# Performance work log

Hardware: AMD Instinct MI355X
Metric: run time of the kernel (lower is better)

Reference implementation:

```python
import jax, jax.numpy as jnp
import numpy as np

DT = 0.01
OMEGA_MAX = 100.0


def setup_inputs() -> dict:
    key = jax.random.key(0)
    ks = jax.random.split(key, 7)
    B, T, D, M = 4, 4096, 1024, 64
    N = 2 * M
    u = jax.random.normal(ks[0], (B, T, D), dtype=jnp.float32)
    W_omega = jax.random.normal(ks[1], (M, D), dtype=jnp.float32) * 0.02
    b_omega = jnp.ones((M,), dtype=jnp.float32)
    W_zeta = jax.random.normal(ks[2], (M, D), dtype=jnp.float32) * 0.02
    b_zeta = jnp.zeros((M,), dtype=jnp.float32)
    W_B = jax.random.normal(ks[3], (N, D), dtype=jnp.float32) * (0.1 / np.sqrt(D))
    b_B = jnp.zeros((N,), dtype=jnp.float32)
    C = jax.random.normal(ks[4], (D, N), dtype=jnp.float32) * 0.01
    D_mat = jax.random.normal(ks[5], (D, D), dtype=jnp.float32) * 0.01
    return dict(u=u, W_omega=W_omega, b_omega=b_omega, W_zeta=W_zeta,
                b_zeta=b_zeta, W_B=W_B, b_B=b_B, C=C, D_mat=D_mat)


def reference(u, W_omega, b_omega, W_zeta, b_zeta, W_B, b_B, C, D_mat):
    B, T, D = u.shape
    M = W_omega.shape[0]
    # Hoist all per-step linear projections into batched GEMMs (same math).
    omega = jax.nn.softplus(jnp.einsum('btd,md->btm', u, W_omega) + b_omega)
    omega = jnp.clip(omega, 1e-4, OMEGA_MAX)                      # (B,T,M)
    zeta = jax.nn.sigmoid(jnp.einsum('btd,md->btm', u, W_zeta) + b_zeta)
    A = omega * omega                                             # (B,T,M)
    S = 1.0 / (1.0 + (DT * DT) * A)                               # (B,T,M)
    d = 1.0 - zeta                                                # (B,T,M)
    F = jnp.einsum('btd,nd->btn', u, W_B) + b_B                   # (B,T,2M)

    def step(x, inp):
        A_t, S_t, d_t, F_t = inp                                  # (B,M)x3, (B,2M)
        z = x[:, :M]
        y = x[:, M:]
        z_new = d_t * (S_t * z - DT * A_t * S_t * y)
        y_new = d_t * (DT * S_t * z + S_t * y)
        x_new = jnp.concatenate([z_new, y_new], axis=-1) + F_t
        return x_new, x_new

    x0 = jnp.zeros((B, 2 * M), dtype=u.dtype)
    tm = lambda a: jnp.swapaxes(a, 0, 1)  # to time-major for scan
    _, xs = jax.lax.scan(step, x0, (tm(A), tm(S), tm(d), tm(F)))
    xs = jnp.swapaxes(xs, 0, 1)                                   # (B,T,2M)
    # Output projection: y_t = x_t C^T + u_t D^T
    y = jnp.einsum('btn,dn->btd', xs, C) + jnp.einsum('bte,de->btd', u, D_mat)
    return y
```

## Files before the change

kernel.cpp:

```cpp
#include <hip/hip_runtime.h>
#include <hip/hip_bf16.h>
#include <math.h>

#define DTC 0.01f

typedef __attribute__((ext_vector_type(8))) short short8;
typedef __attribute__((ext_vector_type(4))) float f32x4;
typedef unsigned short bf16raw;

__device__ __forceinline__ bf16raw f2bf(float f){
  union { unsigned u; float f; } v; v.f = f;
  unsigned r = v.u + 0x7FFF + ((v.u >> 16) & 1u);
  return (bf16raw)(r >> 16);
}

__device__ __forceinline__ short8 ld8f(const float* __restrict__ p){
  float4 a = *(const float4*)p;
  float4 b = *(const float4*)(p + 4);
  short8 r;
  r[0] = (short)f2bf(a.x); r[1] = (short)f2bf(a.y);
  r[2] = (short)f2bf(a.z); r[3] = (short)f2bf(a.w);
  r[4] = (short)f2bf(b.x); r[5] = (short)f2bf(b.y);
  r[6] = (short)f2bf(b.z); r[7] = (short)f2bf(b.w);
  return r;
}

template<int ITERS>
__device__ __forceinline__ void stage_async(const bf16raw* __restrict__ src, long ld,
                                            long row0, int k0, bf16raw* lds,
                                            int wave, int lane){
  int kchunk = (lane & 3) ^ ((lane >> 3) & 3);
#pragma unroll
  for (int i = 0; i < ITERS; ++i){
    int r0 = (wave*ITERS + i) * 16;
    long row = row0 + r0 + (lane >> 2);
    const bf16raw* gp = src + row*ld + k0 + kchunk*8;
    bf16raw* lp = lds + r0*32;
    __builtin_amdgcn_global_load_lds((const __attribute__((address_space(1))) void*)gp,
                                     (__attribute__((address_space(3))) void*)lp,
                                     16, 0, 0);
  }
}

template<int MI, int NI>
__device__ __forceinline__ void mma_tile(const bf16raw* Alds, const bf16raw* Blds,
                                         f32x4 acc[MI][NI], int wm, int wn, int quad, int t16){
  short8 af[MI], bfr[NI];
  int sw = (quad ^ ((t16 >> 1) & 3)) * 8;
#pragma unroll
  for (int mi = 0; mi < MI; ++mi)
    af[mi] = *(const short8*)(Alds + (wm*(MI*16) + mi*16 + t16)*32 + sw);
#pragma unroll
  for (int ni = 0; ni < NI; ++ni)
    bfr[ni] = *(const short8*)(Blds + (wn*(NI*16) + ni*16 + t16)*32 + sw);
#pragma unroll
  for (int mi = 0; mi < MI; ++mi)
#pragma unroll
    for (int ni = 0; ni < NI; ++ni)
      acc[mi][ni] = __builtin_amdgcn_mfma_f32_16x16x32_bf16(af[mi], bfr[ni], acc[mi][ni], 0, 0, 0);
}

extern "C" __global__ void k_prep(const float* __restrict__ u,
    const float* __restrict__ Wom, const float* __restrict__ Wze,
    const float* __restrict__ WB, const float* __restrict__ Cm,
    const float* __restrict__ Dm, bf16raw* __restrict__ u_bf,
    bf16raw* __restrict__ Wcat, bf16raw* __restrict__ C_bf,
    bf16raw* __restrict__ Dm_bf){
  for (long g = (long)blockIdx.x * 256 + threadIdx.x; g < 2277376;
       g += (long)gridDim.x * 256){
    const float* src; bf16raw* dst; long o;
    if      (g < 2097152){ src = u;   dst = u_bf;          o = g; }
    else if (g < 2105344){ src = Wom; dst = Wcat;          o = g - 2097152; }
    else if (g < 2113536){ src = Wze; dst = Wcat + 65536;  o = g - 2105344; }
    else if (g < 2129920){ src = WB;  dst = Wcat + 131072; o = g - 2113536; }
    else if (g < 2146304){ src = Cm;  dst = C_bf;          o = g - 2129920; }
    else                 { src = Dm;  dst = Dm_bf;         o = g - 2146304; }
    *(short8*)(dst + o*8) = ld8f(src + o*8);
  }
}

extern "C" __global__ __launch_bounds__(256, 4) void k_gemm_p(
    const bf16raw* __restrict__ u_bf, const bf16raw* __restrict__ Wcat,
    float* __restrict__ P){
  __shared__ __align__(16) bf16raw Alds[3*64*32];
  __shared__ __align__(16) bf16raw Blds[3*64*32];
  int tid = threadIdx.x, wave = tid >> 6, lane = tid & 63;
  int quad = lane >> 4, t16 = lane & 15;
  int wm = wave >> 1, wn = wave & 1;
  int id  = blockIdx.y * gridDim.x + blockIdx.x;
  int sid = (id & 7) * 128 + (id >> 3);
  long row0 = (long)(sid >> 2) * 64;
  int  col0 = (sid & 3) * 64;
  f32x4 acc[2][2] = {};

  auto stage = [&](int kt, int buf){
    stage_async<1>(u_bf, 1024, row0, kt*32, Alds + buf*(64*32), wave, lane);
    stage_async<1>(Wcat, 1024, col0, kt*32, Blds + buf*(64*32), wave, lane);
  };

  stage(0, 0);
  stage(1, 1);
  int rd = 0;
  for (int s = 0; s < 30; ++s){
    asm volatile("s_waitcnt vmcnt(2)" ::: "memory");
    __builtin_amdgcn_s_barrier();
    __builtin_amdgcn_sched_barrier(0);
    int st = rd >= 1 ? rd - 1 : 2;
    stage(s + 2, st);
    __builtin_amdgcn_s_setprio(1);
    mma_tile<2,2>(Alds + rd*(64*32), Blds + rd*(64*32), acc, wm, wn, quad, t16);
    __builtin_amdgcn_s_setprio(0);
    rd = rd < 2 ? rd + 1 : 0;
  }
  asm volatile("s_waitcnt vmcnt(2)" ::: "memory");
  __builtin_amdgcn_s_barrier();
  __builtin_amdgcn_sched_barrier(0);
  mma_tile<2,2>(Alds + 0*(64*32), Blds + 0*(64*32), acc, wm, wn, quad, t16);
  asm volatile("s_waitcnt vmcnt(0)" ::: "memory");
  __builtin_amdgcn_s_barrier();
  __builtin_amdgcn_sched_barrier(0);
  mma_tile<2,2>(Alds + 1*(64*32), Blds + 1*(64*32), acc, wm, wn, quad, t16);
#pragma unroll
  for (int mi = 0; mi < 2; ++mi)
#pragma unroll
    for (int ni = 0; ni < 2; ++ni)
#pragma unroll
      for (int r = 0; r < 4; ++r){
        long grow = row0 + wm*32 + mi*16 + quad*4 + r;
        int  gcol = col0 + wn*32 + ni*16 + t16;
        P[grow*256 + gcol] = acc[mi][ni][r];
      }
}

extern "C" __global__ __launch_bounds__(256, 2) void k_gemm_out(
    const bf16raw* __restrict__ Xs, const bf16raw* __restrict__ u_bf,
    const bf16raw* __restrict__ C_bf, const bf16raw* __restrict__ Dm_bf,
    float* __restrict__ out){
  __shared__ __align__(16) bf16raw Alds[3*128*32];
  __shared__ __align__(16) bf16raw Blds[3*256*32];
  int tid = threadIdx.x, wave = tid >> 6, lane = tid & 63;
  int quad = lane >> 4, t16 = lane & 15;
  int wm = wave >> 1, wn = wave & 1;
  int id  = blockIdx.y * gridDim.x + blockIdx.x;
  int sid = (id & 7) * 64 + (id >> 3);
  long row0 = (long)(sid >> 2) * 128;
  int  col0 = (sid & 3) * 256;
  f32x4 acc[4][8] = {};

  auto stage = [&](int s, int buf){
    if (s < 4){
      stage_async<2>(Xs,   128, row0, s*32, Alds + buf*(128*32), wave, lane);
      stage_async<4>(C_bf, 128, col0, s*32, Blds + buf*(256*32), wave, lane);
    } else {
      stage_async<2>(u_bf,  1024, row0, (s-4)*32, Alds + buf*(128*32), wave, lane);
      stage_async<4>(Dm_bf, 1024, col0, (s-4)*32, Blds + buf*(256*32), wave, lane);
    }
  };

  stage(0, 0);
  stage(1, 1);
  int rd = 0;
  for (int s = 0; s < 34; ++s){
    asm volatile("s_waitcnt vmcnt(6)" ::: "memory");
    __builtin_amdgcn_s_barrier();
    __builtin_amdgcn_sched_barrier(0);
    int st = rd >= 1 ? rd - 1 : 2;
    stage(s + 2, st);
    __builtin_amdgcn_s_setprio(1);
    mma_tile<4,8>(Alds + rd*(128*32), Blds + rd*(256*32), acc, wm, wn, quad, t16);
    __builtin_amdgcn_s_setprio(0);
    rd = rd < 2 ? rd + 1 : 0;
  }
  asm volatile("s_waitcnt vmcnt(6)" ::: "memory");
  __builtin_amdgcn_s_barrier();
  __builtin_amdgcn_sched_barrier(0);
  mma_tile<4,8>(Alds + 1*(128*32), Blds + 1*(256*32), acc, wm, wn, quad, t16);
  asm volatile("s_waitcnt vmcnt(0)" ::: "memory");
  __builtin_amdgcn_s_barrier();
  __builtin_amdgcn_sched_barrier(0);
  mma_tile<4,8>(Alds + 2*(128*32), Blds + 2*(256*32), acc, wm, wn, quad, t16);
#pragma unroll
  for (int mi = 0; mi < 4; ++mi)
#pragma unroll
    for (int ni = 0; ni < 8; ++ni)
#pragma unroll
      for (int r = 0; r < 4; ++r){
        long grow = row0 + wm*64 + mi*16 + quad*4 + r;
        int  gcol = col0 + wn*128 + ni*16 + t16;
        out[grow*1024 + gcol] = acc[mi][ni][r];
      }
}

extern "C" __global__ __launch_bounds__(256) void k_scanA(
    const float* __restrict__ P, const float* __restrict__ b_om,
    const float* __restrict__ b_ze, const float* __restrict__ b_B,
    float4* __restrict__ CM, float2* __restrict__ CV){
  int tid = threadIdx.x, c = blockIdx.x;
  int b = tid >> 6, m = tid & 63;
  float bo = b_om[m], bz = b_ze[m], bb0 = b_B[m], bb1 = b_B[64 + m];
  const float* row = P + ((size_t)b*4096 + c*8) * 256;
  float m00=1.f, m01=0.f, m10=0.f, m11=0.f, vz=0.f, vy=0.f;
#pragma unroll
  for (int t = 0; t < 8; ++t){
    const float* r = row + t*256;
    float wo = r[m]       + bo;
    float wz = r[64 + m]  + bz;
    float fz = r[128 + m] + bb0;
    float fy = r[192 + m] + bb1;
    float sp = (wo > 20.f) ? wo : log1pf(expf(wo));
    float omega = fminf(fmaxf(sp, 1e-4f), 100.f);
    float A = omega * omega;
    float S = 1.f / (1.f + DTC*DTC*A);
    float zeta = 1.f / (1.f + expf(-wz));
    float p = (1.f - zeta) * S;
    float q = p * DTC * A;
    float nvz = p*vz - q*vy + fz;
    float nvy = DTC*p*vz + p*vy + fy;
    vz = nvz; vy = nvy;
    float n00 = p*m00 - q*m10;
    float n01 = p*m01 - q*m11;
    float n10 = DTC*p*m00 + p*m10;
    float n11 = DTC*p*m01 + p*m11;
    m00=n00; m01=n01; m10=n10; m11=n11;
  }
  CM[(size_t)c*256 + tid] = make_float4(m00, m01, m10, m11);
  CV[(size_t)c*256 + tid] = make_float2(vz, vy);
}

extern "C" __global__ __launch_bounds__(512) void k_scanB(
    const float4* __restrict__ CM, const float2* __restrict__ CV,
    float2* __restrict__ XIn){
  __shared__ float sm[6][512];
  int s = blockIdx.x;
  int c = threadIdx.x;
  float4 Mv = CM[(size_t)c*256 + s];
  float2 Vv = CV[(size_t)c*256 + s];
  float m00=Mv.x, m01=Mv.y, m10=Mv.z, m11=Mv.w, vz=Vv.x, vy=Vv.y;
#pragma unroll
  for (int off = 1; off < 512; off <<= 1){
    sm[0][c]=m00; sm[1][c]=m01; sm[2][c]=m10; sm[3][c]=m11; sm[4][c]=vz; sm[5][c]=vy;
    __syncthreads();
    if (c >= off){
      int p = c - off;
      float e00=sm[0][p], e01=sm[1][p], e10=sm[2][p], e11=sm[3][p];
      float evz=sm[4][p], evy=sm[5][p];
      float n00 = m00*e00 + m01*e10;
      float n01 = m00*e01 + m01*e11;
      float n10 = m10*e00 + m11*e10;
      float n11 = m10*e01 + m11*e11;
      float nvz = m00*evz + m01*evy + vz;
      float nvy = m10*evz + m11*evy + vy;
      m00=n00; m01=n01; m10=n10; m11=n11; vz=nvz; vy=nvy;
    }
    __syncthreads();
  }
  if (c < 511) XIn[(size_t)(c+1)*256 + s] = make_float2(vz, vy);
  if (c == 0)  XIn[s] = make_float2(0.f, 0.f);
}

extern "C" __global__ __launch_bounds__(256) void k_scanC(
    const float* __restrict__ P, const float* __restrict__ b_om,
    const float* __restrict__ b_ze, const float* __restrict__ b_B,
    const float2* __restrict__ XIn, bf16raw* __restrict__ Xs){
  int tid = threadIdx.x, c = blockIdx.x;
  int b = tid >> 6, m = tid & 63;
  float2 x0 = XIn[(size_t)c*256 + tid];
  float xz = x0.x, xy = x0.y;
  float bo = b_om[m], bz = b_ze[m], bb0 = b_B[m], bb1 = b_B[64 + m];
  const float* row = P + ((size_t)b*4096 + c*8) * 256;
  bf16raw* xp = Xs + ((size_t)b*4096 + c*8) * 128 + m;
#pragma unroll
  for (int t = 0; t < 8; ++t){
    const float* r = row + t*256;
    float wo = r[m]       + bo;
    float wz = r[64 + m]  + bz;
    float fz = r[128 + m] + bb0;
    float fy = r[192 + m] + bb1;
    float sp = (wo > 20.f) ? wo : log1pf(expf(wo));
    float omega = fminf(fmaxf(sp, 1e-4f), 100.f);
    float A = omega * omega;
    float S = 1.f / (1.f + DTC*DTC*A);
    float zeta = 1.f / (1.f + expf(-wz));
    float p = (1.f - zeta) * S;
    float q = p * DTC * A;
    float nz = p*xz - q*xy + fz;
    float ny = DTC*p*xz + p*xy + fy;
    xz = nz; xy = ny;
    xp[t*128]      = f2bf(xz);
    xp[t*128 + 64] = f2bf(xy);
  }
}

extern "C" void kernel_launch(void* const* d_in, const int* in_sizes, int n_in,
                              void* d_out, int out_size, void* d_ws, size_t ws_size,
                              hipStream_t stream){
  const float* u   = (const float*)d_in[0];
  const float* Wom = (const float*)d_in[1];
  const float* bom = (const float*)d_in[2];
  const float* Wze = (const float*)d_in[3];
  const float* bze = (const float*)d_in[4];
  const float* WB  = (const float*)d_in[5];
  const float* bB  = (const float*)d_in[6];
  const float* Cm  = (const float*)d_in[7];
  const float* Dm  = (const float*)d_in[8];
  float* out = (float*)d_out;

  char* ws = (char*)d_ws;
  size_t off = 0;
  bf16raw* u_bf  = (bf16raw*)(ws + off); off += (size_t)16777216*2;
  bf16raw* Wcat  = (bf16raw*)(ws + off); off += (size_t)262144*2;
  bf16raw* C_bf  = (bf16raw*)(ws + off); off += (size_t)131072*2;
  bf16raw* Dm_bf = (bf16raw*)(ws + off); off += (size_t)1048576*2;
  float*   P     = (float*)  (ws + off); off += (size_t)16384*256*4;
  bf16raw* Xs    = (bf16raw*)(ws + off); off += (size_t)16384*128*2;
  float4*  CMw   = (float4*) (ws + off); off += (size_t)512*256*16;
  float2*  CVw   = (float2*) (ws + off); off += (size_t)512*256*8;
  float2*  XIn   = (float2*) (ws + off); off += (size_t)512*256*8;

  k_prep    <<<2048, 256, 0, stream>>>(u, Wom, Wze, WB, Cm, Dm, u_bf, Wcat, C_bf, Dm_bf);
  k_gemm_p  <<<dim3(4, 256), 256, 0, stream>>>(u_bf, Wcat, P);
  k_scanA   <<<512, 256, 0, stream>>>(P, bom, bze, bB, CMw, CVw);
  k_scanB   <<<256, 512, 0, stream>>>(CMw, CVw, XIn);
  k_scanC   <<<512, 256, 0, stream>>>(P, bom, bze, bB, XIn, Xs);
  k_gemm_out<<<dim3(4, 128), 256, 0, stream>>>(Xs, u_bf, C_bf, Dm_bf, out);
}
```

Measured before the change: 215.1 us.

## Fuse three scan kernels into one persistent kernel with grid barriers

Merges the chunk-local scan, the cross-chunk prefix scan and the final re-scan into a single 512-block kernel, separated by software grid barriers built on atomic counters that are reset with a memset. The cross-chunk scan now combines pairs of chunks per thread so a 256-thread block covers all 512 chunks. This removes two kernel launches and their inter-kernel gaps. In exchange it relies on all 512 blocks being co-resident on the device, which the launch does not guarantee, and adds spin-wait and memset overhead.

```diff
diff --git a/kernel.cpp b/kernel.cpp
--- a/kernel.cpp
+++ b/kernel.cpp
@@ -191,103 +191,121 @@
       }
 }
 
-extern "C" __global__ __launch_bounds__(256) void k_scanA(
+__device__ __forceinline__ void coef_row(const float* __restrict__ r, int m,
+                                         float bo, float bz, float bb0, float bb1,
+                                         float& p, float& q, float& fz, float& fy){
+  float wo = r[m]       + bo;
+  float wz = r[64 + m]  + bz;
+  fz = r[128 + m] + bb0;
+  fy = r[192 + m] + bb1;
+  float sp = (wo > 20.f) ? wo : log1pf(expf(wo));
+  float omega = fminf(fmaxf(sp, 1e-4f), 100.f);
+  float A = omega * omega;
+  float S = 1.f / (1.f + DTC*DTC*A);
+  float zeta = 1.f / (1.f + expf(-wz));
+  p = (1.f - zeta) * S;
+  q = p * DTC * A;
+}
+
+__device__ __forceinline__ void grid_barrier(unsigned* cnt, unsigned nblk, int tid){
+  __syncthreads();
+  if (tid == 0){
+    __threadfence();
+    atomicAdd(cnt, 1u);
+    while (__hip_atomic_load(cnt, __ATOMIC_ACQUIRE, __HIP_MEMORY_SCOPE_AGENT) < nblk)
+      __builtin_amdgcn_s_sleep(2);
+  }
+  __syncthreads();
+  __threadfence();
+}
+
+extern "C" __global__ __launch_bounds__(256) void k_scan_fused(
     const float* __restrict__ P, const float* __restrict__ b_om,
     const float* __restrict__ b_ze, const float* __restrict__ b_B,
-    float4* __restrict__ CM, float2* __restrict__ CV){
+    float4* __restrict__ CM, float2* __restrict__ CV,
+    float2* __restrict__ XIn, bf16raw* __restrict__ Xs,
+    unsigned* __restrict__ cnt){
+  __shared__ float sm[6][256];
   int tid = threadIdx.x, c = blockIdx.x;
   int b = tid >> 6, m = tid & 63;
   float bo = b_om[m], bz = b_ze[m], bb0 = b_B[m], bb1 = b_B[64 + m];
-  const float* row = P + ((size_t)b*4096 + c*8) * 256;
-  float m00=1.f, m01=0.f, m10=0.f, m11=0.f, vz=0.f, vy=0.f;
-#pragma unroll
-  for (int t = 0; t < 8; ++t){
-    const float* r = row + t*256;
-    float wo = r[m]       + bo;
-    float wz = r[64 + m]  + bz;
-    float fz = r[128 + m] + bb0;
-    float fy = r[192 + m] + bb1;
-    float sp = (wo > 20.f) ? wo : log1pf(expf(wo));
-    float omega = fminf(fmaxf(sp, 1e-4f), 100.f);
-    float A = omega * omega;
-    float S = 1.f / (1.f + DTC*DTC*A);
-    float zeta = 1.f / (1.f + expf(-wz));
-    float p = (1.f - zeta) * S;
-    float q = p * DTC * A;
-    float nvz = p*vz - q*vy + fz;
-    float nvy = DTC*p*vz + p*vy + fy;
-    vz = nvz; vy = nvy;
-    float n00 = p*m00 - q*m10;
-    float n01 = p*m01 - q*m11;
-    float n10 = DTC*p*m00 + p*m10;
-    float n11 = DTC*p*m01 + p*m11;
-    m00=n00; m01=n01; m10=n10; m11=n11;
-  }
-  CM[(size_t)c*256 + tid] = make_float4(m00, m01, m10, m11);
-  CV[(size_t)c*256 + tid] = make_float2(vz, vy);
-}
-
-extern "C" __global__ __launch_bounds__(512) void k_scanB(
-    const float4* __restrict__ CM, const float2* __restrict__ CV,
-    float2* __restrict__ XIn){
-  __shared__ float sm[6][512];
-  int s = blockIdx.x;
-  int c = threadIdx.x;
-  float4 Mv = CM[(size_t)c*256 + s];
-  float2 Vv = CV[(size_t)c*256 + s];
-  float m00=Mv.x, m01=Mv.y, m10=Mv.z, m11=Mv.w, vz=Vv.x, vy=Vv.y;
-#pragma unroll
-  for (int off = 1; off < 512; off <<= 1){
-    sm[0][c]=m00; sm[1][c]=m01; sm[2][c]=m10; sm[3][c]=m11; sm[4][c]=vz; sm[5][c]=vy;
+
+  {
+    const float* row = P + ((size_t)b*4096 + c*8) * 256;
+    float m00=1.f, m01=0.f, m10=0.f, m11=0.f, vz=0.f, vy=0.f;
+#pragma unroll
+    for (int t = 0; t < 8; ++t){
+      float p, q, fz, fy;
+      coef_row(row + t*256, m, bo, bz, bb0, bb1, p, q, fz, fy);
+      float nvz = p*vz - q*vy + fz;
+      float nvy = DTC*p*vz + p*vy + fy;
+      vz = nvz; vy = nvy;
+      float n00 = p*m00 - q*m10;
+      float n01 = p*m01 - q*m11;
+      float n10 = DTC*p*m00 + p*m10;
+      float n11 = DTC*p*m01 + p*m11;
+      m00=n00; m01=n01; m10=n10; m11=n11;
+    }
+    CM[(size_t)c*256 + tid] = make_float4(m00, m01, m10, m11);
+    CV[(size_t)c*256 + tid] = make_float2(vz, vy);
+  }
+
+  grid_barrier(cnt, 512u, tid);
+
+  if (c < 256){
+    int s = c, t = tid;
+    float4 Ma = CM[(size_t)(2*t)*256 + s];   float2 Va = CV[(size_t)(2*t)*256 + s];
+    float4 Mb = CM[(size_t)(2*t+1)*256 + s]; float2 Vb = CV[(size_t)(2*t+1)*256 + s];
+    float m00 = Mb.x*Ma.x + Mb.y*Ma.z;
+    float m01 = Mb.x*Ma.y + Mb.y*Ma.w;
+    float m10 = Mb.z*Ma.x + Mb.w*Ma.z;
+    float m11 = Mb.z*Ma.y + Mb.w*Ma.w;
+    float vz  = Mb.x*Va.x + Mb.y*Va.y + Vb.x;
+    float vy  = Mb.z*Va.x + Mb.w*Va.y + Vb.y;
+#pragma unroll
+    for (int off = 1; off < 256; off <<= 1){
+      sm[0][t]=m00; sm[1][t]=m01; sm[2][t]=m10; sm[3][t]=m11; sm[4][t]=vz; sm[5][t]=vy;
+      __syncthreads();
+      if (t >= off){
+        int p = t - off;
+        float e00=sm[0][p], e01=sm[1][p], e10=sm[2][p], e11=sm[3][p];
+        float evz=sm[4][p], evy=sm[5][p];
+        float n00 = m00*e00 + m01*e10;
+        float n01 = m00*e01 + m01*e11;
+        float n10 = m10*e00 + m11*e10;
+        float n11 = m10*e01 + m11*e11;
+        float nvz = m00*evz + m01*evy + vz;
+        float nvy = m10*evz + m11*evy + vy;
+        m00=n00; m01=n01; m10=n10; m11=n11; vz=nvz; vy=nvy;
+      }
+      __syncthreads();
+    }
+    sm[4][t]=vz; sm[5][t]=vy;
     __syncthreads();
-    if (c >= off){
-      int p = c - off;
-      float e00=sm[0][p], e01=sm[1][p], e10=sm[2][p], e11=sm[3][p];
-      float evz=sm[4][p], evy=sm[5][p];
-      float n00 = m00*e00 + m01*e10;
-      float n01 = m00*e01 + m01*e11;
-      float n10 = m10*e00 + m11*e10;
-      float n11 = m10*e01 + m11*e11;
-      float nvz = m00*evz + m01*evy + vz;
-      float nvy = m10*evz + m11*evy + vy;
-      m00=n00; m01=n01; m10=n10; m11=n11; vz=nvz; vy=nvy;
+    float evz = (t > 0) ? sm[4][t-1] : 0.f;
+    float evy = (t > 0) ? sm[5][t-1] : 0.f;
+    XIn[(size_t)(2*t)*256 + s]   = make_float2(evz, evy);
+    XIn[(size_t)(2*t+1)*256 + s] = make_float2(Ma.x*evz + Ma.y*evy + Va.x,
+                                               Ma.z*evz + Ma.w*evy + Va.y);
+  }
+
+  grid_barrier(cnt + 1, 512u, tid);
+
+  {
+    float2 x0 = XIn[(size_t)c*256 + tid];
+    float xz = x0.x, xy = x0.y;
+    const float* row = P + ((size_t)b*4096 + c*8) * 256;
+    bf16raw* xp = Xs + ((size_t)b*4096 + c*8) * 128 + m;
+#pragma unroll
+    for (int t = 0; t < 8; ++t){
+      float p, q, fz, fy;
+      coef_row(row + t*256, m, bo, bz, bb0, bb1, p, q, fz, fy);
+      float nz = p*xz - q*xy + fz;
+      float ny = DTC*p*xz + p*xy + fy;
+      xz = nz; xy = ny;
+      xp[t*128]      = f2bf(xz);
+      xp[t*128 + 64] = f2bf(xy);
     }
-    __syncthreads();
-  }
-  if (c < 511) XIn[(size_t)(c+1)*256 + s] = make_float2(vz, vy);
-  if (c == 0)  XIn[s] = make_float2(0.f, 0.f);
-}
-
-extern "C" __global__ __launch_bounds__(256) void k_scanC(
-    const float* __restrict__ P, const float* __restrict__ b_om,
-    const float* __restrict__ b_ze, const float* __restrict__ b_B,
-    const float2* __restrict__ XIn, bf16raw* __restrict__ Xs){
-  int tid = threadIdx.x, c = blockIdx.x;
-  int b = tid >> 6, m = tid & 63;
-  float2 x0 = XIn[(size_t)c*256 + tid];
-  float xz = x0.x, xy = x0.y;
-  float bo = b_om[m], bz = b_ze[m], bb0 = b_B[m], bb1 = b_B[64 + m];
-  const float* row = P + ((size_t)b*4096 + c*8) * 256;
-  bf16raw* xp = Xs + ((size_t)b*4096 + c*8) * 128 + m;
-#pragma unroll
-  for (int t = 0; t < 8; ++t){
-    const float* r = row + t*256;
-    float wo = r[m]       + bo;
-    float wz = r[64 + m]  + bz;
-    float fz = r[128 + m] + bb0;
-    float fy = r[192 + m] + bb1;
-    float sp = (wo > 20.f) ? wo : log1pf(expf(wo));
-    float omega = fminf(fmaxf(sp, 1e-4f), 100.f);
-    float A = omega * omega;
-    float S = 1.f / (1.f + DTC*DTC*A);
-    float zeta = 1.f / (1.f + expf(-wz));
-    float p = (1.f - zeta) * S;
-    float q = p * DTC * A;
-    float nz = p*xz - q*xy + fz;
-    float ny = DTC*p*xz + p*xy + fy;
-    xz = nz; xy = ny;
-    xp[t*128]      = f2bf(xz);
-    xp[t*128 + 64] = f2bf(xy);
   }
 }
 
@@ -316,11 +334,11 @@
   float4*  CMw   = (float4*) (ws + off); off += (size_t)512*256*16;
   float2*  CVw   = (float2*) (ws + off); off += (size_t)512*256*8;
   float2*  XIn   = (float2*) (ws + off); off += (size_t)512*256*8;
-
-  k_prep    <<<2048, 256, 0, stream>>>(u, Wom, Wze, WB, Cm, Dm, u_bf, Wcat, C_bf, Dm_bf);
-  k_gemm_p  <<<dim3(4, 256), 256, 0, stream>>>(u_bf, Wcat, P);
-  k_scanA   <<<512, 256, 0, stream>>>(P, bom, bze, bB, CMw, CVw);
-  k_scanB   <<<256, 512, 0, stream>>>(CMw, CVw, XIn);
-  k_scanC   <<<512, 256, 0, stream>>>(P, bom, bze, bB, XIn, Xs);
-  k_gemm_out<<<dim3(4, 128), 256, 0, stream>>>(Xs, u_bf, C_bf, Dm_bf, out);
-}
+  unsigned* cnt  = (unsigned*)(ws + off); off += 256;
+
+  hipMemsetAsync(cnt, 0, 8, stream);
+  k_prep      <<<2048, 256, 0, stream>>>(u, Wom, Wze, WB, Cm, Dm, u_bf, Wcat, C_bf, Dm_bf);
+  k_gemm_p    <<<dim3(4, 256), 256, 0, stream>>>(u_bf, Wcat, P);
+  k_scan_fused<<<512, 256, 0, stream>>>(P, bom, bze, bB, CMw, CVw, XIn, Xs, cnt);
+  k_gemm_out  <<<dim3(4, 128), 256, 0, stream>>>(Xs, u_bf, C_bf, Dm_bf, out);
+}
```

Result: slower. 370.7 us (+72.3%).
